# Kernel tuning notes

Hardware: AMD Instinct MI355X
Metric: run time of the kernel (lower is better)

## Reference

```python
import jax, jax.numpy as jnp
import numpy as np

B, N, NODE, EDGE, H, SK, SV, PK, PV = 1, 512, 256, 128, 8, 16, 16, 4, 4
EPS = 1e-8
SCALAR_SCALE = (3 * SK) ** -0.5          # num_attn_logits=3
POINT_SCALE = (3 * PK * (9.0 / 2.0)) ** -0.5
PAIR_SCALE = 3 ** -0.5


def setup_inputs() -> dict:
    key = jax.random.key(0)
    ks = jax.random.split(key, 16)
    s = 0.02
    return {
        "node": jax.random.normal(ks[0], (B, N, NODE), jnp.float32),
        "edge": jax.random.normal(ks[1], (B, N, N, EDGE), jnp.float32),
        "rotations": jax.random.normal(ks[2], (B, N, 3, 3), jnp.float32),
        "translations": jax.random.normal(ks[3], (B, N, 3), jnp.float32),
        "W_sq": jax.random.normal(ks[4], (NODE, H * SK), jnp.float32) * s,
        "W_sk": jax.random.normal(ks[5], (NODE, H * SK), jnp.float32) * s,
        "W_sv": jax.random.normal(ks[6], (NODE, H * SV), jnp.float32) * s,
        "W_pq": jax.random.normal(ks[7], (NODE, H * PK * 3), jnp.float32) * s,
        "W_pk": jax.random.normal(ks[8], (NODE, H * PK * 3), jnp.float32) * s,
        "W_pv": jax.random.normal(ks[9], (NODE, H * PV * 3), jnp.float32) * s,
        "point_weights": jnp.log(jnp.expm1(jnp.ones((H,), jnp.float32))),  # softplus^-1(1)
        "W_pb": jax.random.normal(ks[10], (EDGE, H), jnp.float32) * s,
        "b_pb": jnp.zeros((H,), jnp.float32),
        "W_out": jax.random.normal(ks[11], (H * (SV + EDGE + PV * 4), NODE), jnp.float32) * s,
        "b_out": jnp.zeros((NODE,), jnp.float32),
    }


def reference(node, edge, rotations, translations, W_sq, W_sk, W_sv, W_pq, W_pk, W_pv,
              point_weights, W_pb, b_pb, W_out, b_out):
    b, n, _ = node.shape
    # scalar q/k/v: (b, n, h, d)
    qs = (node @ W_sq).reshape(b, n, H, SK)
    ks_ = (node @ W_sk).reshape(b, n, H, SK)
    vs = (node @ W_sv).reshape(b, n, H, SV)
    # point q/k/v in local frame: (b, n, h, d, 3) -> rotate + translate into global frame
    t = translations[:, :, None, None, :]  # (b, n, 1, 1, 3)
    qp = jnp.einsum('bnhdc,bnrc->bnhdr', (node @ W_pq).reshape(b, n, H, PK, 3), rotations) + t
    kp = jnp.einsum('bnhdc,bnrc->bnhdr', (node @ W_pk).reshape(b, n, H, PK, 3), rotations) + t
    vp = jnp.einsum('bnhdc,bnrc->bnhdr', (node @ W_pv).reshape(b, n, H, PV, 3), rotations) + t

    # scalar logits (b, h, i, j)
    logits_scalar = jnp.einsum('bihd,bjhd->bhij', qs, ks_) * SCALAR_SCALE
    # pairwise bias (b, h, i, j)
    logits_pair = (jnp.einsum('bijd,dh->bhij', edge, W_pb) + b_pb[None, :, None, None]) * PAIR_SCALE
    # point logits: sum_{d,c} ||q - k||^2 via expansion (avoids (b,i,j,h,d,3) tensor)
    q2 = (qp ** 2).sum((-2, -1)).transpose(0, 2, 1)  # (b, h, i)
    k2 = (kp ** 2).sum((-2, -1)).transpose(0, 2, 1)  # (b, h, j)
    cross = jnp.einsum('bihdc,bjhdc->bhij', qp, kp)
    point_dist = q2[:, :, :, None] + k2[:, :, None, :] - 2.0 * cross  # (b, h, i, j)
    pw = jax.nn.softplus(point_weights)[None, :, None, None]  # (1, h, 1, 1)
    logits_points = -0.5 * (point_dist * pw * POINT_SCALE)

    attn = jax.nn.softmax(logits_scalar + logits_points + logits_pair, axis=-1)  # (b, h, i, j)

    res_scalar = jnp.einsum('bhij,bjhd->bihd', attn, vs).reshape(b, n, H * SV)
    res_pair = jnp.einsum('bhij,bijd->bihd', attn, edge).reshape(b, n, H * EDGE)
    res_pts = jnp.einsum('bhij,bjhdr->bihdr', attn, vp) - t  # back to origin
    res_pts = jnp.einsum('bnhdr,bnrc->bnhdc', res_pts, rotations)  # inverse rotation (R^T)
    res_norm = jnp.sqrt((res_pts ** 2).sum(-1) + EPS)  # (b, n, h, d)

    out = jnp.concatenate([
        res_scalar,
        res_pts.reshape(b, n, H * PV * 3),
        res_norm.reshape(b, n, H * PV),
        res_pair,
    ], axis=-1)
    return out @ W_out + b_out
```

## Files before the change

kernel.cpp:

```cpp
#include <hip/hip_runtime.h>
#include <hip/hip_fp16.h>
#include <math.h>

#define NN 512
#define NODE_D 256
#define EDGE_D 128
#define HN 8

#define SCALAR_SCALE 0.14433756729740643f
#define POINT_SCALE  0.13608276348795434f
#define PAIR_SCALE   0.5773502691896258f

#define OFF_QS   0
#define OFF_KS   65536
#define OFF_VS   131072
#define OFF_VP   196608
#define OFF_QCAT 245760
#define OFF_KCAT 393216
#define OFF_FEAT 540672
#define OFF_PRAW OFF_FEAT
#define OFF_LG16 1196032
#define OFF_OUTP 2244608

__global__ __launch_bounds__(256) void k_projgemm(
    const float* __restrict__ node,
    const float* __restrict__ Wsq, const float* __restrict__ Wsk, const float* __restrict__ Wsv,
    const float* __restrict__ Wpq, const float* __restrict__ Wpk, const float* __restrict__ Wpv,
    float* __restrict__ ws)
{
  __shared__ float As[32 * 33];
  __shared__ float Bs[32 * 36];
  const int t = threadIdx.x;
  const int it = blockIdx.x;
  const int ct = blockIdx.y;

  const float* W; int ncol, col0; float* dst; int ldd, dcol0;
  if (ct < 12) {
    int a = ct >> 2;
    W = (a == 0) ? Wsq : (a == 1) ? Wsk : Wsv;
    ncol = 128; col0 = (ct & 3) * 32;
    dst = ws + ((a == 0) ? OFF_QS : (a == 1) ? OFF_KS : OFF_VS);
    ldd = 128; dcol0 = col0;
  } else {
    int p = ct - 12;
    int a = p / 3, cc = p % 3;
    W = (a == 0) ? Wpq : (a == 1) ? Wpk : Wpv;
    ncol = 96; col0 = cc * 32;
    dst = ws + OFF_PRAW;
    ldd = 288; dcol0 = a * 96 + cc * 32;
  }

  const int row = t & 31, cb = (t >> 5) * 4;
  float4 acc = {0.f, 0.f, 0.f, 0.f};

  for (int kt = 0; kt < 8; ++kt) {
    __syncthreads();
    #pragma unroll
    for (int q = 0; q < 4; ++q) {
      int f = t + q * 256; int r = f >> 5, c = f & 31;
      As[r * 33 + c] = node[(size_t)(it * 32 + r) * 256 + kt * 32 + c];
      Bs[r * 36 + c] = W[(size_t)(kt * 32 + r) * ncol + col0 + c];
    }
    __syncthreads();
    #pragma unroll
    for (int k = 0; k < 32; ++k) {
      float a = As[row * 33 + k];
      float4 b = *(const float4*)&Bs[k * 36 + cb];
      acc.x += a * b.x; acc.y += a * b.y; acc.z += a * b.z; acc.w += a * b.w;
    }
  }
  *(float4*)&dst[(size_t)(it * 32 + row) * ldd + dcol0 + cb] = acc;
}

__global__ __launch_bounds__(256) void k_rot2(
    const float* __restrict__ rotm, const float* __restrict__ trans,
    const float* __restrict__ pw_in, const float* __restrict__ bpb,
    float* __restrict__ ws)
{
  __shared__ float p_l[4][288];
  __shared__ float r_l[4][288];
  __shared__ float q2_l[4][8];
  __shared__ float k2_l[4][8];
  __shared__ float pw_l[8];
  __shared__ float bpb_l[8];
  const int t = threadIdx.x;
  const int n0 = blockIdx.x * 4;
  const float* praw = ws + OFF_PRAW;
  const float* qs_g = ws + OFF_QS;
  const float* ks_g = ws + OFF_KS;

  if (t < 8) {
    float x = pw_in[t];
    pw_l[t] = 0.5f * POINT_SCALE * logf(1.0f + expf(x));
    bpb_l[t] = bpb[t];
  }
  for (int idx = t; idx < 1152; idx += 256) {
    int row = idx / 288, rem = idx % 288;
    p_l[row][rem] = praw[(size_t)(n0 + row) * 288 + rem];
  }
  __syncthreads();

  for (int idx = t; idx < 1152; idx += 256) {
    int row = idx / 288, rem = idx % 288;
    int a = rem / 96, col = rem % 96;
    int rr = col % 3;
    int n = n0 + row;
    const float* R = rotm + (size_t)(n * 3 + rr) * 3;
    const float* P = &p_l[row][a * 96 + (col - rr)];
    float val = P[0] * R[0] + P[1] * R[1] + P[2] * R[2] + trans[n * 3 + rr];
    r_l[row][a * 96 + col] = val;
    if (a == 2) (ws + OFF_VP)[(size_t)n * 96 + col] = val;
  }
  __syncthreads();

  if (t < 64) {
    int row = t >> 4, rem = t & 15;
    int which = rem >> 3, h = rem & 7;
    const float* src = &r_l[row][which * 96 + h * 12];
    float s = 0.f;
    #pragma unroll
    for (int m = 0; m < 12; ++m) s += src[m] * src[m];
    if (which == 0) q2_l[row][h] = s; else k2_l[row][h] = s;
  }
  __syncthreads();

  for (int idx = t; idx < 2304; idx += 256) {
    int side = idx >= 1152;
    int per = idx - side * 1152;
    int row = per / 288, s = per % 288;
    int h = s / 36, e = s % 36;
    int n = n0 + row;
    float val;
    if (!side) {
      val = (e < 16) ? qs_g[(size_t)n * 128 + h * 16 + e] * SCALAR_SCALE
          : (e < 28) ? 2.0f * pw_l[h] * r_l[row][h * 12 + (e - 16)]
          : (e == 32) ? -pw_l[h]
          : (e == 33) ? (bpb_l[h] * PAIR_SCALE - pw_l[h] * q2_l[row][h])
          : 0.f;
      (ws + OFF_QCAT)[(size_t)n * 288 + s] = val;
    } else {
      val = (e < 16) ? ks_g[(size_t)n * 128 + h * 16 + e]
          : (e < 28) ? r_l[row][96 + h * 12 + (e - 16)]
          : (e == 32) ? k2_l[row][h]
          : (e == 33) ? 1.f
          : 0.f;
      (ws + OFF_KCAT)[(size_t)n * 288 + s] = val;
    }
  }
}

__global__ __launch_bounds__(256) void k_S(
    const float* __restrict__ ws_c, __half* __restrict__ lg16)
{
  __shared__ float4 Qt[32 * 36];
  __shared__ float4 Kt[32 * 37];
  __shared__ __half lgst[32 * 32 * 8];
  const int t = threadIdx.x;
  const int it = blockIdx.x, jt = blockIdx.y;
  const float* Qc = ws_c + OFF_QCAT;
  const float* Kc = ws_c + OFF_KCAT;
  const int ti = t >> 4, tj = t & 15;

  for (int hg = 0; hg < 2; ++hg) {
    __syncthreads();
    for (int f = t; f < 1152; f += 256) {
      int row = f / 36, c = f % 36;
      Qt[row * 36 + c] = *(const float4*)&Qc[(size_t)(it * 32 + row) * 288 + hg * 144 + c * 4];
      Kt[row * 37 + c] = *(const float4*)&Kc[(size_t)(jt * 32 + row) * 288 + hg * 144 + c * 4];
    }
    __syncthreads();

    float acc[2][2][4];
    #pragma unroll
    for (int a = 0; a < 2; ++a)
      #pragma unroll
      for (int b = 0; b < 2; ++b)
        #pragma unroll
        for (int h = 0; h < 4; ++h) acc[a][b][h] = 0.f;

    for (int c = 0; c < 9; ++c) {
      #pragma unroll
      for (int hh = 0; hh < 4; ++hh) {
        float4 q0 = Qt[(2 * ti + 0) * 36 + hh * 9 + c];
        float4 q1 = Qt[(2 * ti + 1) * 36 + hh * 9 + c];
        float4 k0 = Kt[(2 * tj + 0) * 37 + hh * 9 + c];
        float4 k1 = Kt[(2 * tj + 1) * 37 + hh * 9 + c];
        acc[0][0][hh] += q0.x * k0.x + q0.y * k0.y + q0.z * k0.z + q0.w * k0.w;
        acc[0][1][hh] += q0.x * k1.x + q0.y * k1.y + q0.z * k1.z + q0.w * k1.w;
        acc[1][0][hh] += q1.x * k0.x + q1.y * k0.y + q1.z * k0.z + q1.w * k0.w;
        acc[1][1][hh] += q1.x * k1.x + q1.y * k1.y + q1.z * k1.z + q1.w * k1.w;
      }
    }
    #pragma unroll
    for (int a = 0; a < 2; ++a)
      #pragma unroll
      for (int b = 0; b < 2; ++b)
        #pragma unroll
        for (int hh = 0; hh < 4; ++hh)
          lgst[((2 * ti + a) * 32 + (2 * tj + b)) * 8 + hg * 4 + hh] = __float2half(acc[a][b][hh]);
  }
  __syncthreads();

  for (int f = t; f < 1024; f += 256) {
    int il = f >> 5, jl = f & 31;
    float4 v = *(const float4*)&lgst[(il * 32 + jl) * 8];
    *(float4*)&lg16[((size_t)(it * 32 + il) * 512 + jt * 32 + jl) * 8] = v;
  }
}

__global__ __launch_bounds__(256) void k_attnfused(
    const float* __restrict__ edge, const float* __restrict__ rotm,
    const float* __restrict__ trans, const float* __restrict__ ws_r,
    const __half* __restrict__ lg16, const float* __restrict__ Wpb,
    float* __restrict__ feat)
{
  __shared__ float smem[10240];
  __shared__ float w_t[8][17];
  __shared__ float lg_t[16][9];
  __shared__ float mh[8], sh[8], resc[8], linv_l[8];
  __shared__ float op_l[96], rp_l[96];

  const int t = threadIdx.x;
  const int i = blockIdx.x;
  const int dq = t & 31, jg = t >> 5;
  const int jrow = t >> 4, sub = t & 15;
  const int hv = dq >> 2;
  const int hp = (dq < 24) ? (dq / 3) : 0;

  const float* eb  = edge + (size_t)i * 512 * 128;
  const float* vsg = ws_r + OFF_VS;
  const float* vpg = ws_r + OFF_VP;

  float wv[8][8];
  #pragma unroll
  for (int dd = 0; dd < 8; ++dd)
    #pragma unroll
    for (int h = 0; h < 8; ++h)
      wv[dd][h] = Wpb[(size_t)(sub * 8 + dd) * 8 + h] * PAIR_SCALE;

  if (t < 8) { mh[t] = -1e30f; sh[t] = 0.f; }

  float4 accp[8];
  #pragma unroll
  for (int h = 0; h < 8; ++h) accp[h] = {0.f, 0.f, 0.f, 0.f};
  float4 accv = {0.f, 0.f, 0.f, 0.f};
  float4 accw = {0.f, 0.f, 0.f, 0.f};

  float (*e_l)[16][132] = (float(*)[16][132])smem;

  #pragma unroll
  for (int p = 0; p < 2; ++p) {
    int f = p * 256 + t, r = f >> 5, g = f & 31;
    *(float4*)&e_l[0][r][g * 4] = *(const float4*)&eb[(size_t)r * 128 + g * 4];
  }
  __syncthreads();

  int cur = 0;
  for (int tile = 0; tile < 32; ++tile) {
    float4 nxt0, nxt1;
    if (tile < 31) {
      const float* ebn = eb + (size_t)(tile + 1) * 16 * 128;
      { int f = t;       int r = f >> 5, g = f & 31; nxt0 = *(const float4*)&ebn[(size_t)r * 128 + g * 4]; }
      { int f = 256 + t; int r = f >> 5, g = f & 31; nxt1 = *(const float4*)&ebn[(size_t)r * 128 + g * 4]; }
    }

    {
      float p8[8] = {0, 0, 0, 0, 0, 0, 0, 0};
      #pragma unroll
      for (int k = 0; k < 2; ++k) {
        float4 e = *(float4*)&e_l[cur][jrow][(sub * 2 + k) * 4];
        #pragma unroll
        for (int h = 0; h < 8; ++h)
          p8[h] += e.x * wv[k * 4 + 0][h] + e.y * wv[k * 4 + 1][h]
                 + e.z * wv[k * 4 + 2][h] + e.w * wv[k * 4 + 3][h];
      }
      #pragma unroll
      for (int m = 1; m <= 8; m <<= 1)
        #pragma unroll
        for (int h = 0; h < 8; ++h) p8[h] += __shfl_xor(p8[h], m);
      if (sub == 0) {
        #pragma unroll
        for (int h = 0; h < 8; ++h) lg_t[jrow][h] = p8[h];
      }
    }
    __syncthreads();

    if (t < 128) {
      const int hS = t >> 4, jS = t & 15;
      float x = lg_t[jS][hS]
              + __half2float(lg16[((size_t)i * 512 + tile * 16 + jS) * 8 + hS]);
      float mt = x;
      #pragma unroll
      for (int s = 8; s; s >>= 1) mt = fmaxf(mt, __shfl_xor(mt, s));
      float mo = mh[hS];
      float mn = fmaxf(mo, mt);
      float w = __expf(x - mn);
      float sw = w;
      #pragma unroll
      for (int s = 8; s; s >>= 1) sw += __shfl_xor(sw, s);
      w_t[hS][jS] = w;
      if (jS == 0) {
        float r = __expf(mo - mn);
        resc[hS] = r;
        mh[hS] = mn;
        sh[hS] = sh[hS] * r + sw;
      }
    }
    __syncthreads();

    {
      #pragma unroll
      for (int h = 0; h < 8; ++h) {
        float r = resc[h];
        accp[h].x *= r; accp[h].y *= r; accp[h].z *= r; accp[h].w *= r;
      }
      {
        float rv = resc[hv];
        accv.x *= rv; accv.y *= rv; accv.z *= rv; accv.w *= rv;
      }
      if (dq < 24) {
        float rp = resc[hp];
        accw.x *= rp; accw.y *= rp; accw.z *= rp; accw.w *= rp;
      }
      #pragma unroll
      for (int jj = 0; jj < 2; ++jj) {
        int j = jg * 2 + jj;
        float4 e = *(float4*)&e_l[cur][j][dq * 4];
        float wj[8];
        #pragma unroll
        for (int h = 0; h < 8; ++h) wj[h] = w_t[h][j];
        #pragma unroll
        for (int h = 0; h < 8; ++h) {
          accp[h].x += wj[h] * e.x; accp[h].y += wj[h] * e.y;
          accp[h].z += wj[h] * e.z; accp[h].w += wj[h] * e.w;
        }
        int gj = tile * 16 + j;
        float4 v = *(const float4*)&vsg[(size_t)gj * 128 + dq * 4];
        float wvv = wj[hv];
        accv.x += wvv * v.x; accv.y += wvv * v.y;
        accv.z += wvv * v.z; accv.w += wvv * v.w;
        if (dq < 24) {
          float4 pv = *(const float4*)&vpg[(size_t)gj * 96 + dq * 4];
          float wpp = wj[hp];
          accw.x += wpp * pv.x; accw.y += wpp * pv.y;
          accw.z += wpp * pv.z; accw.w += wpp * pv.w;
        }
      }
    }
    __syncthreads();

    if (tile < 31) {
      { int f = t;       int r = f >> 5, g = f & 31; *(float4*)&e_l[cur ^ 1][r][g * 4] = nxt0; }
      { int f = 256 + t; int r = f >> 5, g = f & 31; *(float4*)&e_l[cur ^ 1][r][g * 4] = nxt1; }
      cur ^= 1;
      __syncthreads();
    }
  }

  float* pl  = smem;
  float* vsp = smem + 8448;
  float* vpp = smem + 8448 + 1024;
  {
    #pragma unroll
    for (int h = 0; h < 8; ++h)
      *(float4*)&pl[(size_t)(jg * 8 + h) * 132 + dq * 4] = accp[h];
    *(float4*)&vsp[jg * 128 + dq * 4] = accv;
    if (dq < 24) *(float4*)&vpp[jg * 96 + dq * 4] = accw;
  }
  if (t < 8) linv_l[t] = 1.0f / sh[t];
  __syncthreads();

  float* frow = feat + (size_t)i * 1280;

  {
    const int h = t >> 5, d4 = (t & 31) * 4;
    float4 s = {0.f, 0.f, 0.f, 0.f};
    #pragma unroll
    for (int q = 0; q < 8; ++q) {
      float4 v = *(const float4*)&pl[(size_t)(q * 8 + h) * 132 + d4];
      s.x += v.x; s.y += v.y; s.z += v.z; s.w += v.w;
    }
    float li = linv_l[h];
    s.x *= li; s.y *= li; s.z *= li; s.w *= li;
    *(float4*)&frow[256 + h * 128 + d4] = s;
  }
  if (t < 128) {
    float s = 0.f;
    #pragma unroll
    for (int q = 0; q < 8; ++q) s += vsp[q * 128 + t];
    frow[t] = s * linv_l[t >> 4];
  }
  if (t < 96) {
    float s = 0.f;
    #pragma unroll
    for (int q = 0; q < 8; ++q) s += vpp[q * 96 + t];
    op_l[t] = s * linv_l[t / 12] - trans[i * 3 + (t % 3)];
  }
  __syncthreads();

  if (t < 96) {
    int c = t % 3, base = t - c;
    const float* R = rotm + (size_t)i * 9;
    float val = op_l[base] * R[c] + op_l[base + 1] * R[3 + c] + op_l[base + 2] * R[6 + c];
    rp_l[t] = val;
    frow[128 + t] = val;
  }
  __syncthreads();
  if (t < 32) {
    float x = rp_l[t * 3], y = rp_l[t * 3 + 1], z = rp_l[t * 3 + 2];
    frow[224 + t] = sqrtf(x * x + y * y + z * z + 1e-8f);
  }
}

__global__ __launch_bounds__(256) void k_outp(
    const float* __restrict__ feat, const float* __restrict__ Wout,
    float* __restrict__ ws)
{
  __shared__ float As[32 * 33];
  __shared__ float Bs[32 * 36];
  const int t = threadIdx.x;
  const int it = blockIdx.x, ot = blockIdx.y, z = blockIdx.z;
  const int row = t & 31, cb = (t >> 5) * 4;
  float4 acc = {0.f, 0.f, 0.f, 0.f};

  for (int kk = 0; kk < 10; ++kk) {
    int kt = z * 10 + kk;
    __syncthreads();
    #pragma unroll
    for (int q = 0; q < 4; ++q) {
      int f = t + q * 256; int r = f >> 5, c = f & 31;
      As[r * 33 + c] = feat[(size_t)(it * 32 + r) * 1280 + kt * 32 + c];
      Bs[r * 36 + c] = Wout[(size_t)(kt * 32 + r) * 256 + ot * 32 + c];
    }
    __syncthreads();
    #pragma unroll
    for (int k = 0; k < 32; ++k) {
      float a = As[row * 33 + k];
      float4 bv = *(const float4*)&Bs[k * 36 + cb];
      acc.x += a * bv.x; acc.y += a * bv.y; acc.z += a * bv.z; acc.w += a * bv.w;
    }
  }
  float* pc = ws + OFF_OUTP + (size_t)z * 131072;
  *(float4*)&pc[(size_t)(it * 32 + row) * 256 + ot * 32 + cb] = acc;
}

__global__ __launch_bounds__(256) void k_outr(
    const float* __restrict__ ws, const float* __restrict__ bout,
    float* __restrict__ out)
{
  const int q = blockIdx.x * 256 + threadIdx.x;
  const float* pc = ws + OFF_OUTP;
  float4 a = *(const float4*)&pc[(size_t)q * 4];
  float4 b = *(const float4*)&pc[(size_t)q * 4 + 131072];
  float4 c = *(const float4*)&pc[(size_t)q * 4 + 262144];
  float4 d = *(const float4*)&pc[(size_t)q * 4 + 393216];
  float4 bias = *(const float4*)&bout[(q & 63) * 4];
  float4 r;
  r.x = a.x + b.x + c.x + d.x + bias.x;
  r.y = a.y + b.y + c.y + d.y + bias.y;
  r.z = a.z + b.z + c.z + d.z + bias.z;
  r.w = a.w + b.w + c.w + d.w + bias.w;
  *(float4*)&out[(size_t)q * 4] = r;
}

extern "C" void kernel_launch(void* const* d_in, const int* in_sizes, int n_in,
                              void* d_out, int out_size, void* d_ws, size_t ws_size,
                              hipStream_t stream) {
  const float* node  = (const float*)d_in[0];
  const float* edge  = (const float*)d_in[1];
  const float* rotm  = (const float*)d_in[2];
  const float* trans = (const float*)d_in[3];
  const float* Wsq   = (const float*)d_in[4];
  const float* Wsk   = (const float*)d_in[5];
  const float* Wsv   = (const float*)d_in[6];
  const float* Wpq   = (const float*)d_in[7];
  const float* Wpk   = (const float*)d_in[8];
  const float* Wpv   = (const float*)d_in[9];
  const float* pw    = (const float*)d_in[10];
  const float* Wpb   = (const float*)d_in[11];
  const float* bpb   = (const float*)d_in[12];
  const float* Wout  = (const float*)d_in[13];
  const float* bout  = (const float*)d_in[14];
  float* ws   = (float*)d_ws;
  float* out  = (float*)d_out;
  float* feat = ws + OFF_FEAT;
  __half* lg16 = (__half*)(ws + OFF_LG16);

  k_projgemm<<<dim3(16, 21), 256, 0, stream>>>(node, Wsq, Wsk, Wsv, Wpq, Wpk, Wpv, ws);
  k_rot2<<<128, 256, 0, stream>>>(rotm, trans, pw, bpb, ws);
  k_S<<<dim3(16, 16), 256, 0, stream>>>(ws, lg16);
  k_attnfused<<<512, 256, 0, stream>>>(edge, rotm, trans, ws, lg16, Wpb, feat);
  k_outp<<<dim3(16, 8, 4), 256, 0, stream>>>(feat, Wout, ws);
  k_outr<<<128, 256, 0, stream>>>(ws, bout, out);
}
```

Baseline: 128.8 us.

## Split attention over key halves with flash-decoding style partial merge

The fused attention kernel now splits each query row's 512 keys into two chunks of 256 handled by separate blocks (1024 blocks instead of 512). Each block writes its partial max, sum and accumulators, and a new merge kernel rescales and combines them before the point-frame transforms. Tiles also grow from 16 to 32 keys, halving the loop iterations and barriers per block and using all 256 threads for the softmax step. This costs an extra kernel launch, a partial-result round trip through global memory, and more shared memory per block.

```diff
diff --git a/kernel.cpp b/kernel.cpp
--- a/kernel.cpp
+++ b/kernel.cpp
@@ -21,6 +21,7 @@
 #define OFF_PRAW OFF_FEAT
 #define OFF_LG16 1196032
 #define OFF_OUTP 2244608
+#define OFF_PART 2768896
 
 __global__ __launch_bounds__(256) void k_projgemm(
     const float* __restrict__ node,
@@ -208,28 +209,30 @@
   }
 }
 
-__global__ __launch_bounds__(256) void k_attnfused(
-    const float* __restrict__ edge, const float* __restrict__ rotm,
-    const float* __restrict__ trans, const float* __restrict__ ws_r,
+__global__ __launch_bounds__(256) void k_attnfused2(
+    const float* __restrict__ edge, const float* __restrict__ ws_r,
     const __half* __restrict__ lg16, const float* __restrict__ Wpb,
-    float* __restrict__ feat)
-{
-  __shared__ float smem[10240];
-  __shared__ float w_t[8][17];
-  __shared__ float lg_t[16][9];
-  __shared__ float mh[8], sh[8], resc[8], linv_l[8];
-  __shared__ float op_l[96], rp_l[96];
+    float* __restrict__ part)
+{
+  __shared__ float e_l[2][32][132];
+  __shared__ float w_t[8][33];
+  __shared__ float lg_t[32][9];
+  __shared__ float mh[8], sh[8], resc[8];
+  __shared__ float vsp[4 * 128];
+  __shared__ float vpp[4 * 96];
 
   const int t = threadIdx.x;
-  const int i = blockIdx.x;
+  const int jc = blockIdx.x;
+  const int i  = blockIdx.y;
   const int dq = t & 31, jg = t >> 5;
-  const int jrow = t >> 4, sub = t & 15;
+  const int sub = t & 15;
   const int hv = dq >> 2;
   const int hp = (dq < 24) ? (dq / 3) : 0;
 
-  const float* eb  = edge + (size_t)i * 512 * 128;
-  const float* vsg = ws_r + OFF_VS;
-  const float* vpg = ws_r + OFF_VP;
+  const float* eb  = edge + ((size_t)i * 512 + jc * 256) * 128;
+  const float* vsg = ws_r + OFF_VS + (size_t)jc * 256 * 128;
+  const float* vpg = ws_r + OFF_VP + (size_t)jc * 256 * 96;
+  const __half* lgb = lg16 + ((size_t)i * 512 + jc * 256) * 8;
 
   float wv[8][8];
   #pragma unroll
@@ -246,25 +249,27 @@
   float4 accv = {0.f, 0.f, 0.f, 0.f};
   float4 accw = {0.f, 0.f, 0.f, 0.f};
 
-  float (*e_l)[16][132] = (float(*)[16][132])smem;
-
   #pragma unroll
-  for (int p = 0; p < 2; ++p) {
+  for (int p = 0; p < 4; ++p) {
     int f = p * 256 + t, r = f >> 5, g = f & 31;
     *(float4*)&e_l[0][r][g * 4] = *(const float4*)&eb[(size_t)r * 128 + g * 4];
   }
   __syncthreads();
 
   int cur = 0;
-  for (int tile = 0; tile < 32; ++tile) {
-    float4 nxt0, nxt1;
-    if (tile < 31) {
-      const float* ebn = eb + (size_t)(tile + 1) * 16 * 128;
-      { int f = t;       int r = f >> 5, g = f & 31; nxt0 = *(const float4*)&ebn[(size_t)r * 128 + g * 4]; }
-      { int f = 256 + t; int r = f >> 5, g = f & 31; nxt1 = *(const float4*)&ebn[(size_t)r * 128 + g * 4]; }
-    }
-
-    {
+  for (int tile = 0; tile < 8; ++tile) {
+    float4 nxt0, nxt1, nxt2, nxt3;
+    if (tile < 7) {
+      const float* ebn = eb + (size_t)(tile + 1) * 32 * 128;
+      { int f = t;           int r = f >> 5, g = f & 31; nxt0 = *(const float4*)&ebn[(size_t)r * 128 + g * 4]; }
+      { int f = 256 + t;     int r = f >> 5, g = f & 31; nxt1 = *(const float4*)&ebn[(size_t)r * 128 + g * 4]; }
+      { int f = 512 + t;     int r = f >> 5, g = f & 31; nxt2 = *(const float4*)&ebn[(size_t)r * 128 + g * 4]; }
+      { int f = 768 + t;     int r = f >> 5, g = f & 31; nxt3 = *(const float4*)&ebn[(size_t)r * 128 + g * 4]; }
+    }
+
+    #pragma unroll
+    for (int pass = 0; pass < 2; ++pass) {
+      const int jrow = (t >> 4) + pass * 16;
       float p8[8] = {0, 0, 0, 0, 0, 0, 0, 0};
       #pragma unroll
       for (int k = 0; k < 2; ++k) {
@@ -285,19 +290,19 @@
     }
     __syncthreads();
 
-    if (t < 128) {
-      const int hS = t >> 4, jS = t & 15;
+    {
+      const int hS = t >> 5, jS = t & 31;
       float x = lg_t[jS][hS]
-              + __half2float(lg16[((size_t)i * 512 + tile * 16 + jS) * 8 + hS]);
+              + __half2float(lgb[(size_t)(tile * 32 + jS) * 8 + hS]);
       float mt = x;
       #pragma unroll
-      for (int s = 8; s; s >>= 1) mt = fmaxf(mt, __shfl_xor(mt, s));
+      for (int s = 16; s; s >>= 1) mt = fmaxf(mt, __shfl_xor(mt, s));
       float mo = mh[hS];
       float mn = fmaxf(mo, mt);
       float w = __expf(x - mn);
       float sw = w;
       #pragma unroll
-      for (int s = 8; s; s >>= 1) sw += __shfl_xor(sw, s);
+      for (int s = 16; s; s >>= 1) sw += __shfl_xor(sw, s);
       w_t[hS][jS] = w;
       if (jS == 0) {
         float r = __expf(mo - mn);
@@ -323,8 +328,8 @@
         accw.x *= rp; accw.y *= rp; accw.z *= rp; accw.w *= rp;
       }
       #pragma unroll
-      for (int jj = 0; jj < 2; ++jj) {
-        int j = jg * 2 + jj;
+      for (int jj = 0; jj < 4; ++jj) {
+        const int j = jg * 4 + jj;
         float4 e = *(float4*)&e_l[cur][j][dq * 4];
         float wj[8];
         #pragma unroll
@@ -334,7 +339,7 @@
           accp[h].x += wj[h] * e.x; accp[h].y += wj[h] * e.y;
           accp[h].z += wj[h] * e.z; accp[h].w += wj[h] * e.w;
         }
-        int gj = tile * 16 + j;
+        const int gj = tile * 32 + j;
         float4 v = *(const float4*)&vsg[(size_t)gj * 128 + dq * 4];
         float wvv = wj[hv];
         accv.x += wvv * v.x; accv.y += wvv * v.y;
@@ -349,52 +354,97 @@
     }
     __syncthreads();
 
-    if (tile < 31) {
+    if (tile < 7) {
       { int f = t;       int r = f >> 5, g = f & 31; *(float4*)&e_l[cur ^ 1][r][g * 4] = nxt0; }
       { int f = 256 + t; int r = f >> 5, g = f & 31; *(float4*)&e_l[cur ^ 1][r][g * 4] = nxt1; }
+      { int f = 512 + t; int r = f >> 5, g = f & 31; *(float4*)&e_l[cur ^ 1][r][g * 4] = nxt2; }
+      { int f = 768 + t; int r = f >> 5, g = f & 31; *(float4*)&e_l[cur ^ 1][r][g * 4] = nxt3; }
       cur ^= 1;
       __syncthreads();
     }
   }
 
-  float* pl  = smem;
-  float* vsp = smem + 8448;
-  float* vpp = smem + 8448 + 1024;
-  {
+  #pragma unroll
+  for (int h = 0; h < 8; ++h) {
+    accp[h].x += __shfl_xor(accp[h].x, 32);
+    accp[h].y += __shfl_xor(accp[h].y, 32);
+    accp[h].z += __shfl_xor(accp[h].z, 32);
+    accp[h].w += __shfl_xor(accp[h].w, 32);
+  }
+  accv.x += __shfl_xor(accv.x, 32); accv.y += __shfl_xor(accv.y, 32);
+  accv.z += __shfl_xor(accv.z, 32); accv.w += __shfl_xor(accv.w, 32);
+  accw.x += __shfl_xor(accw.x, 32); accw.y += __shfl_xor(accw.y, 32);
+  accw.z += __shfl_xor(accw.z, 32); accw.w += __shfl_xor(accw.w, 32);
+
+  const int wid = t >> 6;
+  float* pl = (float*)e_l;
+  if ((t & 63) < 32) {
     #pragma unroll
     for (int h = 0; h < 8; ++h)
-      *(float4*)&pl[(size_t)(jg * 8 + h) * 132 + dq * 4] = accp[h];
-    *(float4*)&vsp[jg * 128 + dq * 4] = accv;
-    if (dq < 24) *(float4*)&vpp[jg * 96 + dq * 4] = accw;
-  }
-  if (t < 8) linv_l[t] = 1.0f / sh[t];
-  __syncthreads();
-
-  float* frow = feat + (size_t)i * 1280;
-
+      *(float4*)&pl[(size_t)(wid * 8 + h) * 132 + dq * 4] = accp[h];
+    *(float4*)&vsp[wid * 128 + dq * 4] = accv;
+    if (dq < 24) *(float4*)&vpp[wid * 96 + dq * 4] = accw;
+  }
+  __syncthreads();
+
+  float* pp = part + ((size_t)i * 2 + jc) * 1280;
+  if (t < 8) { pp[t] = mh[t]; pp[8 + t] = sh[t]; }
   {
     const int h = t >> 5, d4 = (t & 31) * 4;
     float4 s = {0.f, 0.f, 0.f, 0.f};
     #pragma unroll
-    for (int q = 0; q < 8; ++q) {
-      float4 v = *(const float4*)&pl[(size_t)(q * 8 + h) * 132 + d4];
+    for (int q = 0; q < 4; ++q) {
+      float4 v = *(float4*)&pl[(size_t)(q * 8 + h) * 132 + d4];
       s.x += v.x; s.y += v.y; s.z += v.z; s.w += v.w;
     }
-    float li = linv_l[h];
-    s.x *= li; s.y *= li; s.z *= li; s.w *= li;
-    *(float4*)&frow[256 + h * 128 + d4] = s;
+    *(float4*)&pp[16 + h * 128 + d4] = s;
+  }
+  if (t < 128)
+    pp[1040 + t] = vsp[t] + vsp[128 + t] + vsp[256 + t] + vsp[384 + t];
+  if (t < 96)
+    pp[1168 + t] = vpp[t] + vpp[96 + t] + vpp[192 + t] + vpp[288 + t];
+}
+
+__global__ __launch_bounds__(256) void k_amerge(
+    const float* __restrict__ part, const float* __restrict__ rotm,
+    const float* __restrict__ trans, float* __restrict__ feat)
+{
+  __shared__ float r0s[8], r1s[8], lis[8];
+  __shared__ float op_l[96], rp_l[96];
+  const int t = threadIdx.x, i = blockIdx.x;
+  const float* p0 = part + (size_t)i * 2560;
+  const float* p1 = p0 + 1280;
+
+  if (t < 8) {
+    float m0 = p0[t], m1 = p1[t];
+    float M = fmaxf(m0, m1);
+    float r0 = __expf(m0 - M), r1 = __expf(m1 - M);
+    float S = p0[8 + t] * r0 + p1[8 + t] * r1;
+    r0s[t] = r0; r1s[t] = r1; lis[t] = 1.0f / S;
+  }
+  __syncthreads();
+
+  float* frow = feat + (size_t)i * 1280;
+  {
+    const int h = t >> 5, d4 = (t & 31) * 4;
+    float4 a = *(const float4*)&p0[16 + h * 128 + d4];
+    float4 b = *(const float4*)&p1[16 + h * 128 + d4];
+    float r0 = r0s[h], r1 = r1s[h], li = lis[h];
+    float4 o;
+    o.x = (a.x * r0 + b.x * r1) * li;
+    o.y = (a.y * r0 + b.y * r1) * li;
+    o.z = (a.z * r0 + b.z * r1) * li;
+    o.w = (a.w * r0 + b.w * r1) * li;
+    *(float4*)&frow[256 + h * 128 + d4] = o;
   }
   if (t < 128) {
-    float s = 0.f;
-    #pragma unroll
-    for (int q = 0; q < 8; ++q) s += vsp[q * 128 + t];
-    frow[t] = s * linv_l[t >> 4];
+    int h = t >> 4;
+    frow[t] = (p0[1040 + t] * r0s[h] + p1[1040 + t] * r1s[h]) * lis[h];
   }
   if (t < 96) {
-    float s = 0.f;
-    #pragma unroll
-    for (int q = 0; q < 8; ++q) s += vpp[q * 96 + t];
-    op_l[t] = s * linv_l[t / 12] - trans[i * 3 + (t % 3)];
+    int h = t / 12;
+    op_l[t] = (p0[1168 + t] * r0s[h] + p1[1168 + t] * r1s[h]) * lis[h]
+            - trans[i * 3 + (t % 3)];
   }
   __syncthreads();
 
@@ -485,11 +535,13 @@
   float* out  = (float*)d_out;
   float* feat = ws + OFF_FEAT;
   __half* lg16 = (__half*)(ws + OFF_LG16);
+  float* part = ws + OFF_PART;
 
   k_projgemm<<<dim3(16, 21), 256, 0, stream>>>(node, Wsq, Wsk, Wsv, Wpq, Wpk, Wpv, ws);
   k_rot2<<<128, 256, 0, stream>>>(rotm, trans, pw, bpb, ws);
   k_S<<<dim3(16, 16), 256, 0, stream>>>(ws, lg16);
-  k_attnfused<<<512, 256, 0, stream>>>(edge, rotm, trans, ws, lg16, Wpb, feat);
+  k_attnfused2<<<dim3(2, 512), 256, 0, stream>>>(edge, ws, lg16, Wpb, part);
+  k_amerge<<<512, 256, 0, stream>>>(part, rotm, trans, feat);
   k_outp<<<dim3(16, 8, 4), 256, 0, stream>>>(feat, Wout, ws);
   k_outr<<<128, 256, 0, stream>>>(ws, bout, out);
 }
```

After: 128.4 us. Within noise of the previous version (-0.3%).
